# Performance work log

Measured on AMD Instinct MI355X. Metric: run time of the kernel, lower is better.

Reference implementation:

```python
import jax, jax.numpy as jnp
import numpy as np
import math

N_NODES = 100000
N_EDGES = 1600000
DIM = 64


def setup_inputs() -> dict:
    key = jax.random.key(0)
    ks = jax.random.split(key, 16)
    s = 1.0 / math.sqrt(DIM)
    inp = {
        "x": jax.random.normal(ks[0], (N_NODES, DIM), jnp.float32),
        "edge_vec": jax.random.normal(ks[1], (N_EDGES, 3), jnp.float32),
        # lin_Q / lin_K / lin_V
        "Wq": jax.random.normal(ks[2], (DIM, DIM), jnp.float32) * s,
        "bq": jnp.zeros((DIM,), jnp.float32),
        "Wk": jax.random.normal(ks[3], (DIM, DIM), jnp.float32) * s,
        "bk": jnp.zeros((DIM,), jnp.float32),
        "Wv": jax.random.normal(ks[4], (DIM, DIM), jnp.float32) * s,
        "bv": jnp.zeros((DIM,), jnp.float32),
        # edge_bias MLP: [4 -> dim -> dim -> 1], SiLU between layers
        "W1": jax.random.normal(ks[5], (4, DIM), jnp.float32) * 0.5,
        "b1": jnp.zeros((DIM,), jnp.float32),
        "W2": jax.random.normal(ks[6], (DIM, DIM), jnp.float32) * s,
        "b2": jnp.zeros((DIM,), jnp.float32),
        "W3": jax.random.normal(ks[7], (DIM, 1), jnp.float32) * s,
        "b3": jnp.zeros((1,), jnp.float32),
        # w_F
        "wF": jax.random.normal(ks[8], (DIM, 1), jnp.float32) * s,
        "bF": jnp.zeros((1,), jnp.float32),
        "edge_index": jax.random.randint(ks[9], (2, N_EDGES), 0, N_NODES, jnp.int32),
    }
    return inp


def reference(x, edge_vec, Wq, bq, Wk, bk, Wv, bv, W1, b1, W2, b2, W3, b3, wF, bF, edge_index):
    n = x.shape[0]
    dim = x.shape[1]
    i = edge_index[0]
    j = edge_index[1]

    # project on nodes (N << E), then gather to edges
    query = (x @ Wq + bq)[j]          # [E, dim]
    key = (x @ Wk + bk)[i]            # [E, dim]
    value = (x @ Wv + bv)[i]          # [E, dim]

    # edge MLP bias on [vec, |vec|]
    edge_len = jnp.linalg.norm(edge_vec, axis=-1, keepdims=True)  # [E, 1]
    edge_attr = jnp.concatenate([edge_vec, edge_len], axis=-1)    # [E, 4]
    h = jax.nn.silu(edge_attr @ W1 + b1)
    h = jax.nn.silu(h @ W2 + b2)
    bias = (h @ W3 + b3)[:, 0]        # [E]

    scores = jnp.sum(query * key, axis=-1) / jnp.sqrt(jnp.asarray(dim, x.dtype)) + bias  # [E]

    # segment softmax over target node j
    smax = jax.ops.segment_max(scores, j, num_segments=n)
    smax = jnp.where(jnp.isfinite(smax), smax, 0.0)
    ex = jnp.exp(scores - smax[j])
    denom = jax.ops.segment_sum(ex, j, num_segments=n)
    alpha = ex / (denom[j] + 1e-16)   # [E]

    # scatter-weighted vector aggregation
    gate = value @ wF + bF            # [E, 1]
    vec_out = jax.ops.segment_sum(alpha[:, None] * gate * edge_vec, j, num_segments=n)  # [N, 3]
    return vec_out
```

## Files before the change

### kernel.cpp

```cpp
#include <hip/hip_runtime.h>
#include <hip/hip_bf16.h>
#include <math.h>

#define DIM 64

typedef __attribute__((ext_vector_type(8))) short bf16x8;
typedef __attribute__((ext_vector_type(4))) float f32x4;
typedef unsigned short ushort_t;

__device__ __forceinline__ float silu_f(float x) {
    float e = __expf(-x);
    return x * __builtin_amdgcn_rcpf(1.0f + e);
}
__device__ __forceinline__ unsigned short f2bf_fast(float x) {
    unsigned u = __builtin_bit_cast(unsigned, x);
    u += 0x7FFFu + ((u >> 16) & 1u);
    return (unsigned short)(u >> 16);
}

__global__ __launch_bounds__(256) void k_proj_mfma(
    const float* __restrict__ x,
    const float* __restrict__ Wq, const float* __restrict__ bq,
    const float* __restrict__ Wk, const float* __restrict__ bk,
    const float* __restrict__ Wv, const float* __restrict__ bv,
    const float* __restrict__ wF, const float* __restrict__ bF,
    ushort_t* __restrict__ Qh, ushort_t* __restrict__ Kh,
    float* __restrict__ gate, float* __restrict__ out4,
    int nNodes, int nTiles)
{
    const int tid = threadIdx.x;
    const int lane = tid & 63;
    const int w = tid >> 6;
    const int lanen = lane & 15;
    const int q = lane >> 4;

    float accu = 0.f;
    #pragma unroll
    for (int n = 0; n < 64; ++n) accu = fmaf(Wv[lane * 64 + n], wF[n], accu);
    float pc = bv[lane] * wF[lane];
    #pragma unroll
    for (int off = 32; off; off >>= 1) pc += __shfl_xor(pc, off, 64);
    const float c0 = pc + bF[0];
    const int ubits = __builtin_bit_cast(int, accu);
    float ur0[8], ur1[8];
    #pragma unroll
    for (int j = 0; j < 8; ++j) {
        ur0[j] = __builtin_bit_cast(float, __builtin_amdgcn_ds_bpermute((q * 8 + j) * 4, ubits));
        ur1[j] = __builtin_bit_cast(float, __builtin_amdgcn_ds_bpermute((32 + q * 8 + j) * 4, ubits));
    }

    bf16x8 Bq[2][4], Bk[2][4];
    #pragma unroll
    for (int c = 0; c < 2; ++c)
        #pragma unroll
        for (int t = 0; t < 4; ++t) {
            bf16x8 vq, vk;
            #pragma unroll
            for (int j = 0; j < 8; ++j) {
                int idx = (c * 32 + q * 8 + j) * 64 + t * 16 + lanen;
                vq[j] = (short)f2bf_fast(Wq[idx]);
                vk[j] = (short)f2bf_fast(Wk[idx]);
            }
            Bq[c][t] = vq; Bk[c][t] = vk;
        }
    float bqv[4], bkv[4];
    #pragma unroll
    for (int t = 0; t < 4; ++t) { bqv[t] = bq[t * 16 + lanen]; bkv[t] = bk[t * 16 + lanen]; }

    const int waveId = blockIdx.x * 4 + w;
    const int wstride = gridDim.x * 4;

    for (int tile = waveId; tile < nTiles; tile += wstride) {
        int node0 = tile * 16;
        int nodeA = node0 + lanen;
        int nodeC = (nodeA < nNodes) ? nodeA : (nNodes - 1);
        const float4* xr = (const float4*)(x + (size_t)nodeC * 64);
        float4 xa = xr[q * 2], xb = xr[q * 2 + 1];
        float4 xc = xr[8 + q * 2], xd = xr[8 + q * 2 + 1];

        float g = xa.x * ur0[0] + xa.y * ur0[1] + xa.z * ur0[2] + xa.w * ur0[3]
                + xb.x * ur0[4] + xb.y * ur0[5] + xb.z * ur0[6] + xb.w * ur0[7]
                + xc.x * ur1[0] + xc.y * ur1[1] + xc.z * ur1[2] + xc.w * ur1[3]
                + xd.x * ur1[4] + xd.y * ur1[5] + xd.z * ur1[6] + xd.w * ur1[7];
        g += __shfl_xor(g, 16);
        g += __shfl_xor(g, 32);

        bf16x8 a0, a1;
        a0[0] = (short)f2bf_fast(xa.x); a0[1] = (short)f2bf_fast(xa.y);
        a0[2] = (short)f2bf_fast(xa.z); a0[3] = (short)f2bf_fast(xa.w);
        a0[4] = (short)f2bf_fast(xb.x); a0[5] = (short)f2bf_fast(xb.y);
        a0[6] = (short)f2bf_fast(xb.z); a0[7] = (short)f2bf_fast(xb.w);
        a1[0] = (short)f2bf_fast(xc.x); a1[1] = (short)f2bf_fast(xc.y);
        a1[2] = (short)f2bf_fast(xc.z); a1[3] = (short)f2bf_fast(xc.w);
        a1[4] = (short)f2bf_fast(xd.x); a1[5] = (short)f2bf_fast(xd.y);
        a1[6] = (short)f2bf_fast(xd.z); a1[7] = (short)f2bf_fast(xd.w);

        f32x4 accq[4] = {{0,0,0,0},{0,0,0,0},{0,0,0,0},{0,0,0,0}};
        f32x4 acck[4] = {{0,0,0,0},{0,0,0,0},{0,0,0,0},{0,0,0,0}};
        #pragma unroll
        for (int t = 0; t < 4; ++t) {
            accq[t] = __builtin_amdgcn_mfma_f32_16x16x32_bf16(a0, Bq[0][t], accq[t], 0, 0, 0);
            accq[t] = __builtin_amdgcn_mfma_f32_16x16x32_bf16(a1, Bq[1][t], accq[t], 0, 0, 0);
            acck[t] = __builtin_amdgcn_mfma_f32_16x16x32_bf16(a0, Bk[0][t], acck[t], 0, 0, 0);
            acck[t] = __builtin_amdgcn_mfma_f32_16x16x32_bf16(a1, Bk[1][t], acck[t], 0, 0, 0);
        }

        #pragma unroll
        for (int t = 0; t < 4; ++t)
            #pragma unroll
            for (int r = 0; r < 4; ++r) {
                int node = node0 + q * 4 + r;
                if (node < nNodes) {
                    size_t o = (size_t)node * 64 + t * 16 + lanen;
                    Qh[o] = f2bf_fast(accq[t][r] + bqv[t]);
                    Kh[o] = f2bf_fast(acck[t][r] + bkv[t]);
                }
            }
        if (nodeA < nNodes) {
            if (q == 0) gate[nodeA] = g + c0;
            if (q == 1) *(float4*)(out4 + (size_t)nodeA * 4) = make_float4(0.f, 0.f, 0.f, 0.f);
        }
    }
}

__global__ __launch_bounds__(256) void k_edge_mfma(
    const int* __restrict__ ei, const int* __restrict__ ej,
    const ushort_t* __restrict__ Qh, const ushort_t* __restrict__ Kh,
    const float* __restrict__ gate, const float* __restrict__ edge_vec,
    const float* __restrict__ W1, const float* __restrict__ b1,
    const float* __restrict__ W2, const float* __restrict__ b2,
    const float* __restrict__ W3, const float* __restrict__ b3,
    float* __restrict__ out4, int nEdges, long nTiles)
{
    __shared__ __align__(16) float4 sW1v[72];
    __shared__ float sB1[64];

    const int tid = threadIdx.x;
    const int lane = tid & 63;
    const int lanen = lane & 15;
    const int q = lane >> 4;
    const int w = tid >> 6;

    if (tid < 64) {
        int slot = tid + (tid >> 3);
        sW1v[slot] = make_float4(W1[tid], W1[64 + tid], W1[128 + tid], W1[192 + tid]);
        sB1[tid] = b1[tid];
    }

    bf16x8 Bfrag[2][4];
    #pragma unroll
    for (int c = 0; c < 2; ++c)
        #pragma unroll
        for (int t = 0; t < 4; ++t) {
            bf16x8 v;
            #pragma unroll
            for (int j = 0; j < 8; ++j)
                v[j] = (short)f2bf_fast(W2[(c * 32 + q * 8 + j) * 64 + t * 16 + lanen]);
            Bfrag[c][t] = v;
        }
    float b2r[4], w3r[4];
    #pragma unroll
    for (int t = 0; t < 4; ++t) { b2r[t] = b2[t * 16 + lanen]; w3r[t] = W3[t * 16 + lanen]; }
    const float b3r = b3[0];
    const int rsel = lanen & 3;
    const int bperm_addr = ((((lanen >> 2) << 4) | lanen) << 2);
    __syncthreads();

    const long wstride = (long)gridDim.x * 4;
    const long t0 = (long)blockIdx.x * 4 + w;

    auto idx_of = [&](long tile, int& ii, int& jj) {
        long es = tile * 16 + lanen;
        long esc = (es < nEdges) ? es : (long)(nEdges - 1);
        ii = ei[esc]; jj = ej[esc];
    };
    auto gather = [&](long tile, int ii, int jj,
                      bf16x8& A, bf16x8& B, bf16x8& C, bf16x8& D, float& G, float4& AT) {
        const bf16x8* qp = (const bf16x8*)(Qh + (size_t)jj * 64);
        A = qp[q]; B = qp[4 + q];
        const bf16x8* kp = (const bf16x8*)(Kh + (size_t)ii * 64);
        C = kp[q]; D = kp[4 + q];
        G = gate[ii];
        long em = tile * 16 + lanen;
        long emc = (em < nEdges) ? em : (long)(nEdges - 1);
        float ax = edge_vec[emc * 3 + 0];
        float ay = edge_vec[emc * 3 + 1];
        float az = edge_vec[emc * 3 + 2];
        AT = make_float4(ax, ay, az, sqrtf(ax * ax + ay * ay + az * az));
    };

    int iC, jC, iN, jN;
    idx_of(t0, iC, jC);
    idx_of(t0 + wstride, iN, jN);
    bf16x8 qa = {}, qb = {}, ka = {}, kb = {};
    float gte = 0.f;
    float4 attr = make_float4(0.f, 0.f, 0.f, 0.f);
    gather(t0, iC, jC, qa, qb, ka, kb, gte, attr);

    for (long tile = t0; tile < nTiles; tile += wstride) {
        int pw0[4], pw1[4];
        #pragma unroll
        for (int jj = 0; jj < 4; ++jj) {
            int d0 = q * 8 + 2 * jj;
            float4 cA = sW1v[d0 + q];
            float4 cB = sW1v[d0 + 1 + q];
            float4 cC = sW1v[d0 + 32 + q + 4];
            float4 cD = sW1v[d0 + 33 + q + 4];
            float p0 = sB1[d0]      + attr.x*cA.x + attr.y*cA.y + attr.z*cA.z + attr.w*cA.w;
            float p1 = sB1[d0 + 1]  + attr.x*cB.x + attr.y*cB.y + attr.z*cB.z + attr.w*cB.w;
            float p2 = sB1[d0 + 32] + attr.x*cC.x + attr.y*cC.y + attr.z*cC.z + attr.w*cC.w;
            float p3 = sB1[d0 + 33] + attr.x*cD.x + attr.y*cD.y + attr.z*cD.z + attr.w*cD.w;
            float h0 = silu_f(p0), h1v = silu_f(p1), h2v = silu_f(p2), h3v = silu_f(p3);
            int r0, r1;
            asm("v_cvt_pk_bf16_f32 %0, %1, %2" : "=v"(r0) : "v"(h0), "v"(h1v));
            asm("v_cvt_pk_bf16_f32 %0, %1, %2" : "=v"(r1) : "v"(h2v), "v"(h3v));
            pw0[jj] = r0; pw1[jj] = r1;
        }
        bf16x8 a0 = __builtin_bit_cast(bf16x8, make_int4(pw0[0], pw0[1], pw0[2], pw0[3]));
        bf16x8 a1 = __builtin_bit_cast(bf16x8, make_int4(pw1[0], pw1[1], pw1[2], pw1[3]));

        f32x4 accd = {0.f, 0.f, 0.f, 0.f};
        accd = __builtin_amdgcn_mfma_f32_16x16x32_bf16(qa, ka, accd, 0, 0, 0);
        accd = __builtin_amdgcn_mfma_f32_16x16x32_bf16(qb, kb, accd, 0, 0, 0);

        f32x4 acc[4] = {{0,0,0,0},{0,0,0,0},{0,0,0,0},{0,0,0,0}};
        #pragma unroll
        for (int t = 0; t < 4; ++t) {
            acc[t] = __builtin_amdgcn_mfma_f32_16x16x32_bf16(a0, Bfrag[0][t], acc[t], 0, 0, 0);
            acc[t] = __builtin_amdgcn_mfma_f32_16x16x32_bf16(a1, Bfrag[1][t], acc[t], 0, 0, 0);
        }

        int iF, jF;
        idx_of(tile + 2 * wstride, iF, jF);
        bf16x8 qa2 = {}, qb2 = {}, ka2 = {}, kb2 = {};
        float gte2 = 0.f;
        float4 attr2 = make_float4(0.f, 0.f, 0.f, 0.f);
        gather(tile + wstride, iN, jN, qa2, qb2, ka2, kb2, gte2, attr2);

        float part[4] = {0.f, 0.f, 0.f, 0.f};
        #pragma unroll
        for (int t = 0; t < 4; ++t)
            #pragma unroll
            for (int r = 0; r < 4; ++r)
                part[r] += silu_f(acc[t][r] + b2r[t]) * w3r[t];
        #pragma unroll
        for (int r = 0; r < 4; ++r) {
            part[r] += __shfl_xor(part[r], 1);
            part[r] += __shfl_xor(part[r], 2);
            part[r] += __shfl_xor(part[r], 4);
            part[r] += __shfl_xor(part[r], 8);
        }

        float dsel = accd[0];
        dsel = (rsel == 1) ? accd[1] : dsel;
        dsel = (rsel == 2) ? accd[2] : dsel;
        dsel = (rsel == 3) ? accd[3] : dsel;
        float psel = part[0];
        psel = (rsel == 1) ? part[1] : psel;
        psel = (rsel == 2) ? part[2] : psel;
        psel = (rsel == 3) ? part[3] : psel;
        float val = fmaf(dsel, 0.125f, psel);
        int moved = __builtin_amdgcn_ds_bpermute(bperm_addr, __builtin_bit_cast(int, val));
        float sc = __builtin_bit_cast(float, moved) + b3r;

        float ev = __expf(sc);
        long eC = tile * 16 + lanen;
        if (eC < nEdges) {
            float comp = (q == 0) ? attr.x : (q == 1) ? attr.y : attr.z;
            float vout = (q == 3) ? ev : ev * gte * comp;
            atomicAdd(out4 + (size_t)jC * 4 + q, vout);
        }

        iC = iN; jC = jN; iN = iF; jN = jF;
        qa = qa2; qb = qb2; ka = ka2; kb = kb2; gte = gte2; attr = attr2;
    }
}

__global__ __launch_bounds__(256) void k_div(
    const float4* __restrict__ out4, float* __restrict__ out, int nNodes)
{
    int j = blockIdx.x * 256 + threadIdx.x;
    if (j >= nNodes) return;
    float4 v = out4[j];
    float inv = 1.0f / (v.w + 1e-16f);
    out[(size_t)j * 3 + 0] = v.x * inv;
    out[(size_t)j * 3 + 1] = v.y * inv;
    out[(size_t)j * 3 + 2] = v.z * inv;
}

extern "C" void kernel_launch(void* const* d_in, const int* in_sizes, int n_in,
                              void* d_out, int out_size, void* d_ws, size_t ws_size,
                              hipStream_t stream)
{
    const float* x        = (const float*)d_in[0];
    const float* edge_vec = (const float*)d_in[1];
    const float* Wq = (const float*)d_in[2];
    const float* bq = (const float*)d_in[3];
    const float* Wk = (const float*)d_in[4];
    const float* bk = (const float*)d_in[5];
    const float* Wv = (const float*)d_in[6];
    const float* bv = (const float*)d_in[7];
    const float* W1 = (const float*)d_in[8];
    const float* b1 = (const float*)d_in[9];
    const float* W2 = (const float*)d_in[10];
    const float* b2 = (const float*)d_in[11];
    const float* W3 = (const float*)d_in[12];
    const float* b3 = (const float*)d_in[13];
    const float* wF = (const float*)d_in[14];
    const float* bF = (const float*)d_in[15];
    const int*   eidx = (const int*)d_in[16];

    int nNodes = in_sizes[0] / DIM;
    int nEdges = in_sizes[16] / 2;
    const int* ei = eidx;
    const int* ej = eidx + nEdges;

    char* p = (char*)d_ws;
    ushort_t* Qh = (ushort_t*)p;
    ushort_t* Kh = Qh + (size_t)nNodes * DIM;
    p += (size_t)nNodes * DIM * 2 * sizeof(ushort_t);
    float* gate = (float*)p;  p += (size_t)nNodes * sizeof(float);
    float* out4 = (float*)p;  p += (size_t)nNodes * 4 * sizeof(float);

    float* out = (float*)d_out;

    int nTilesN = (nNodes + 15) / 16;
    k_proj_mfma<<<1024, 256, 0, stream>>>(x, Wq, bq, Wk, bk, Wv, bv, wF, bF,
                                          Qh, Kh, gate, out4, nNodes, nTilesN);

    long nTilesE = (nEdges + 15) / 16;
    k_edge_mfma<<<2048, 256, 0, stream>>>(ei, ej, Qh, Kh, gate, edge_vec,
                                          W1, b1, W2, b2, W3, b3,
                                          out4, nEdges, nTilesE);

    int nBn = (nNodes + 255) / 256;
    k_div<<<nBn, 256, 0, stream>>>((const float4*)out4, out, nNodes);
}
```

Measured before the change: 239.9 us.

## Vectorize projection stores, use packed FP32 math, swizzle reductions and MFMA priority

The projection kernel swaps MFMA operand order so each lane holds 4 contiguous output columns of one node. This lets it add bias with packed adds and write 8-byte bf16 stores instead of scattered 2-byte stores. The edge kernel recomputes the first MLP layer with v_pk_fma_f32 on a re-laid-out W1 in LDS, adds bias with packed adds, and replaces shfl_xor reductions with ds_swizzle. Both kernels also raise wave priority around the MFMA blocks. Together these aim to cut VALU instruction count and store transactions, at the cost of inline-asm complexity.

```diff
diff --git a/kernel.cpp b/kernel.cpp
--- a/kernel.cpp
+++ b/kernel.cpp
@@ -6,6 +6,7 @@
 
 typedef __attribute__((ext_vector_type(8))) short bf16x8;
 typedef __attribute__((ext_vector_type(4))) float f32x4;
+typedef __attribute__((ext_vector_type(2))) float f32x2;
 typedef unsigned short ushort_t;
 
 __device__ __forceinline__ float silu_f(float x) {
@@ -16,6 +17,33 @@
     unsigned u = __builtin_bit_cast(unsigned, x);
     u += 0x7FFFu + ((u >> 16) & 1u);
     return (unsigned short)(u >> 16);
+}
+__device__ __forceinline__ unsigned cvtpk_bf16(float a, float b) {
+    unsigned r;
+    asm("v_cvt_pk_bf16_f32 %0, %1, %2" : "=v"(r) : "v"(a), "v"(b));
+    return r;
+}
+__device__ __forceinline__ f32x2 pk_fma2(f32x2 a, f32x2 b, f32x2 c) {
+    f32x2 d;
+    asm("v_pk_fma_f32 %0, %1, %2, %3" : "=v"(d) : "v"(a), "v"(b), "v"(c));
+    return d;
+}
+__device__ __forceinline__ f32x2 pk_add2(f32x2 a, f32x2 b) {
+    f32x2 d;
+    asm("v_pk_add_f32 %0, %1, %2" : "=v"(d) : "v"(a), "v"(b));
+    return d;
+}
+__device__ __forceinline__ f32x2 bc2(float x) { f32x2 r; r.x = x; r.y = x; return r; }
+__device__ __forceinline__ float swz_add(float v, const int pat) {
+    int iv = __builtin_bit_cast(int, v);
+    int sv;
+    switch (pat) {
+        case 1: sv = __builtin_amdgcn_ds_swizzle(iv, 0x041F); break;
+        case 2: sv = __builtin_amdgcn_ds_swizzle(iv, 0x081F); break;
+        case 4: sv = __builtin_amdgcn_ds_swizzle(iv, 0x101F); break;
+        default: sv = __builtin_amdgcn_ds_swizzle(iv, 0x201F); break;
+    }
+    return v + __builtin_bit_cast(float, sv);
 }
 
 __global__ __launch_bounds__(256) void k_proj_mfma(
@@ -63,9 +91,11 @@
             }
             Bq[c][t] = vq; Bk[c][t] = vk;
         }
-    float bqv[4], bkv[4];
-    #pragma unroll
-    for (int t = 0; t < 4; ++t) { bqv[t] = bq[t * 16 + lanen]; bkv[t] = bk[t * 16 + lanen]; }
+    const float4* bq4p = (const float4*)bq;
+    const float4* bk4p = (const float4*)bk;
+    float4 bq4[4], bk4[4];
+    #pragma unroll
+    for (int t = 0; t < 4; ++t) { bq4[t] = bq4p[t * 4 + q]; bk4[t] = bk4p[t * 4 + q]; }
 
     const int waveId = blockIdx.x * 4 + w;
     const int wstride = gridDim.x * 4;
@@ -97,26 +127,34 @@
 
         f32x4 accq[4] = {{0,0,0,0},{0,0,0,0},{0,0,0,0},{0,0,0,0}};
         f32x4 acck[4] = {{0,0,0,0},{0,0,0,0},{0,0,0,0},{0,0,0,0}};
-        #pragma unroll
-        for (int t = 0; t < 4; ++t) {
-            accq[t] = __builtin_amdgcn_mfma_f32_16x16x32_bf16(a0, Bq[0][t], accq[t], 0, 0, 0);
-            accq[t] = __builtin_amdgcn_mfma_f32_16x16x32_bf16(a1, Bq[1][t], accq[t], 0, 0, 0);
-            acck[t] = __builtin_amdgcn_mfma_f32_16x16x32_bf16(a0, Bk[0][t], acck[t], 0, 0, 0);
-            acck[t] = __builtin_amdgcn_mfma_f32_16x16x32_bf16(a1, Bk[1][t], acck[t], 0, 0, 0);
-        }
-
-        #pragma unroll
-        for (int t = 0; t < 4; ++t)
+        __builtin_amdgcn_s_setprio(1);
+        #pragma unroll
+        for (int t = 0; t < 4; ++t) {
+            accq[t] = __builtin_amdgcn_mfma_f32_16x16x32_bf16(Bq[0][t], a0, accq[t], 0, 0, 0);
+            accq[t] = __builtin_amdgcn_mfma_f32_16x16x32_bf16(Bq[1][t], a1, accq[t], 0, 0, 0);
+            acck[t] = __builtin_amdgcn_mfma_f32_16x16x32_bf16(Bk[0][t], a0, acck[t], 0, 0, 0);
+            acck[t] = __builtin_amdgcn_mfma_f32_16x16x32_bf16(Bk[1][t], a1, acck[t], 0, 0, 0);
+        }
+        __builtin_amdgcn_s_setprio(0);
+
+        if (nodeA < nNodes) {
+            ushort_t* qrow = Qh + (size_t)nodeA * 64 + q * 4;
+            ushort_t* krow = Kh + (size_t)nodeA * 64 + q * 4;
             #pragma unroll
-            for (int r = 0; r < 4; ++r) {
-                int node = node0 + q * 4 + r;
-                if (node < nNodes) {
-                    size_t o = (size_t)node * 64 + t * 16 + lanen;
-                    Qh[o] = f2bf_fast(accq[t][r] + bqv[t]);
-                    Kh[o] = f2bf_fast(acck[t][r] + bkv[t]);
-                }
+            for (int t = 0; t < 4; ++t) {
+                f32x2 q01 = pk_add2((f32x2){accq[t][0], accq[t][1]}, (f32x2){bq4[t].x, bq4[t].y});
+                f32x2 q23 = pk_add2((f32x2){accq[t][2], accq[t][3]}, (f32x2){bq4[t].z, bq4[t].w});
+                uint2 pq;
+                pq.x = cvtpk_bf16(q01.x, q01.y);
+                pq.y = cvtpk_bf16(q23.x, q23.y);
+                *(uint2*)(qrow + t * 16) = pq;
+                f32x2 k01 = pk_add2((f32x2){acck[t][0], acck[t][1]}, (f32x2){bk4[t].x, bk4[t].y});
+                f32x2 k23 = pk_add2((f32x2){acck[t][2], acck[t][3]}, (f32x2){bk4[t].z, bk4[t].w});
+                uint2 pk;
+                pk.x = cvtpk_bf16(k01.x, k01.y);
+                pk.y = cvtpk_bf16(k23.x, k23.y);
+                *(uint2*)(krow + t * 16) = pk;
             }
-        if (nodeA < nNodes) {
             if (q == 0) gate[nodeA] = g + c0;
             if (q == 1) *(float4*)(out4 + (size_t)nodeA * 4) = make_float4(0.f, 0.f, 0.f, 0.f);
         }
@@ -132,8 +170,8 @@
     const float* __restrict__ W3, const float* __restrict__ b3,
     float* __restrict__ out4, int nEdges, long nTiles)
 {
-    __shared__ __align__(16) float4 sW1v[72];
-    __shared__ float sB1[64];
+    __shared__ __align__(16) float4 sW1x[72];
+    __shared__ __align__(8) f32x2 sB1p[32];
 
     const int tid = threadIdx.x;
     const int lane = tid & 63;
@@ -142,9 +180,15 @@
     const int w = tid >> 6;
 
     if (tid < 64) {
-        int slot = tid + (tid >> 3);
-        sW1v[slot] = make_float4(W1[tid], W1[64 + tid], W1[128 + tid], W1[192 + tid]);
-        sB1[tid] = b1[tid];
+        int pp = tid >> 1, hh = tid & 1;
+        int d0 = pp * 2, k0 = hh * 2;
+        sW1x[tid + (tid >> 3)] = make_float4(
+            W1[k0 * 64 + d0], W1[k0 * 64 + d0 + 1],
+            W1[(k0 + 1) * 64 + d0], W1[(k0 + 1) * 64 + d0 + 1]);
+    }
+    if (tid < 32) {
+        f32x2 bp; bp.x = b1[2 * tid]; bp.y = b1[2 * tid + 1];
+        sB1p[tid] = bp;
     }
 
     bf16x8 Bfrag[2][4];
@@ -159,11 +203,18 @@
             Bfrag[c][t] = v;
         }
     float b2r[4], w3r[4];
-    #pragma unroll
-    for (int t = 0; t < 4; ++t) { b2r[t] = b2[t * 16 + lanen]; w3r[t] = W3[t * 16 + lanen]; }
+    f32x2 b2p[4];
+    #pragma unroll
+    for (int t = 0; t < 4; ++t) {
+        b2r[t] = b2[t * 16 + lanen];
+        w3r[t] = W3[t * 16 + lanen];
+        b2p[t] = bc2(b2r[t]);
+    }
     const float b3r = b3[0];
     const int rsel = lanen & 3;
     const int bperm_addr = ((((lanen >> 2) << 4) | lanen) << 2);
+    const int slotA0 = q * 9;
+    const int slotB0 = 36 + q * 9;
     __syncthreads();
 
     const long wstride = (long)gridDim.x * 4;
@@ -198,37 +249,41 @@
     gather(t0, iC, jC, qa, qb, ka, kb, gte, attr);
 
     for (long tile = t0; tile < nTiles; tile += wstride) {
+        f32x2 ax2 = bc2(attr.x), ay2 = bc2(attr.y), az2 = bc2(attr.z), aw2 = bc2(attr.w);
         int pw0[4], pw1[4];
         #pragma unroll
-        for (int jj = 0; jj < 4; ++jj) {
-            int d0 = q * 8 + 2 * jj;
-            float4 cA = sW1v[d0 + q];
-            float4 cB = sW1v[d0 + 1 + q];
-            float4 cC = sW1v[d0 + 32 + q + 4];
-            float4 cD = sW1v[d0 + 33 + q + 4];
-            float p0 = sB1[d0]      + attr.x*cA.x + attr.y*cA.y + attr.z*cA.z + attr.w*cA.w;
-            float p1 = sB1[d0 + 1]  + attr.x*cB.x + attr.y*cB.y + attr.z*cB.z + attr.w*cB.w;
-            float p2 = sB1[d0 + 32] + attr.x*cC.x + attr.y*cC.y + attr.z*cC.z + attr.w*cC.w;
-            float p3 = sB1[d0 + 33] + attr.x*cD.x + attr.y*cD.y + attr.z*cD.z + attr.w*cD.w;
-            float h0 = silu_f(p0), h1v = silu_f(p1), h2v = silu_f(p2), h3v = silu_f(p3);
-            int r0, r1;
-            asm("v_cvt_pk_bf16_f32 %0, %1, %2" : "=v"(r0) : "v"(h0), "v"(h1v));
-            asm("v_cvt_pk_bf16_f32 %0, %1, %2" : "=v"(r1) : "v"(h2v), "v"(h3v));
-            pw0[jj] = r0; pw1[jj] = r1;
+        for (int s = 0; s < 4; ++s) {
+            float4 wa0 = sW1x[slotA0 + 2 * s];
+            float4 wa1 = sW1x[slotA0 + 2 * s + 1];
+            f32x2 hA = sB1p[q * 4 + s];
+            hA = pk_fma2((f32x2){wa0.x, wa0.y}, ax2, hA);
+            hA = pk_fma2((f32x2){wa0.z, wa0.w}, ay2, hA);
+            hA = pk_fma2((f32x2){wa1.x, wa1.y}, az2, hA);
+            hA = pk_fma2((f32x2){wa1.z, wa1.w}, aw2, hA);
+            float4 wb0 = sW1x[slotB0 + 2 * s];
+            float4 wb1 = sW1x[slotB0 + 2 * s + 1];
+            f32x2 hB = sB1p[16 + q * 4 + s];
+            hB = pk_fma2((f32x2){wb0.x, wb0.y}, ax2, hB);
+            hB = pk_fma2((f32x2){wb0.z, wb0.w}, ay2, hB);
+            hB = pk_fma2((f32x2){wb1.x, wb1.y}, az2, hB);
+            hB = pk_fma2((f32x2){wb1.z, wb1.w}, aw2, hB);
+            pw0[s] = (int)cvtpk_bf16(silu_f(hA.x), silu_f(hA.y));
+            pw1[s] = (int)cvtpk_bf16(silu_f(hB.x), silu_f(hB.y));
         }
         bf16x8 a0 = __builtin_bit_cast(bf16x8, make_int4(pw0[0], pw0[1], pw0[2], pw0[3]));
         bf16x8 a1 = __builtin_bit_cast(bf16x8, make_int4(pw1[0], pw1[1], pw1[2], pw1[3]));
 
+        __builtin_amdgcn_s_setprio(1);
         f32x4 accd = {0.f, 0.f, 0.f, 0.f};
         accd = __builtin_amdgcn_mfma_f32_16x16x32_bf16(qa, ka, accd, 0, 0, 0);
         accd = __builtin_amdgcn_mfma_f32_16x16x32_bf16(qb, kb, accd, 0, 0, 0);
-
         f32x4 acc[4] = {{0,0,0,0},{0,0,0,0},{0,0,0,0},{0,0,0,0}};
         #pragma unroll
         for (int t = 0; t < 4; ++t) {
             acc[t] = __builtin_amdgcn_mfma_f32_16x16x32_bf16(a0, Bfrag[0][t], acc[t], 0, 0, 0);
             acc[t] = __builtin_amdgcn_mfma_f32_16x16x32_bf16(a1, Bfrag[1][t], acc[t], 0, 0, 0);
         }
+        __builtin_amdgcn_s_setprio(0);
 
         int iF, jF;
         idx_of(tile + 2 * wstride, iF, jF);
@@ -239,16 +294,20 @@
 
         float part[4] = {0.f, 0.f, 0.f, 0.f};
         #pragma unroll
-        for (int t = 0; t < 4; ++t)
-            #pragma unroll
-            for (int r = 0; r < 4; ++r)
-                part[r] += silu_f(acc[t][r] + b2r[t]) * w3r[t];
+        for (int t = 0; t < 4; ++t) {
+            f32x2 s01 = pk_add2((f32x2){acc[t][0], acc[t][1]}, b2p[t]);
+            f32x2 s23 = pk_add2((f32x2){acc[t][2], acc[t][3]}, b2p[t]);
+            part[0] = fmaf(silu_f(s01.x), w3r[t], part[0]);
+            part[1] = fmaf(silu_f(s01.y), w3r[t], part[1]);
+            part[2] = fmaf(silu_f(s23.x), w3r[t], part[2]);
+            part[3] = fmaf(silu_f(s23.y), w3r[t], part[3]);
+        }
         #pragma unroll
         for (int r = 0; r < 4; ++r) {
-            part[r] += __shfl_xor(part[r], 1);
-            part[r] += __shfl_xor(part[r], 2);
-            part[r] += __shfl_xor(part[r], 4);
-            part[r] += __shfl_xor(part[r], 8);
+            part[r] = swz_add(part[r], 1);
+            part[r] = swz_add(part[r], 2);
+            part[r] = swz_add(part[r], 4);
+            part[r] = swz_add(part[r], 8);
         }
 
         float dsel = accd[0];
```

Result: faster. 233.3 us (-2.7%).
